# Kernel tuning notes

Measured on AMD Instinct MI355X. Metric: run time of the kernel, lower is better.

Reference implementation:

```python
import jax, jax.numpy as jnp
import numpy as np

MARGIN = 0.2
BATCH = 512
FEAT = 256
NUM_CLASSES = 64


def setup_inputs() -> dict:
    key = jax.random.key(0)
    k1, k2 = jax.random.split(key)
    inputs = jax.random.normal(k1, (BATCH, FEAT), dtype=jnp.float32)
    y = jax.random.randint(k2, (BATCH,), 0, NUM_CLASSES, dtype=jnp.int64)
    return {"inputs": inputs, "y": y}


def reference(inputs, y):
    b = y.shape[0]
    # pairwise squared distances: |x_i|^2 + |x_j|^2 - 2 x_i . x_j
    gram = inputs @ inputs.T                      # [B, B]
    sq = jnp.diagonal(gram)                       # [B]
    pdist = sq[:, None] + sq[None, :] - 2.0 * gram  # [B, B]

    # validity mask over (i, j, k): i!=j, i!=k, j!=k, y_i==y_j, y_i!=y_k
    not_eq = 1.0 - jnp.eye(b, dtype=inputs.dtype)           # [B, B]
    eq_label = (y[None, :] == y[:, None]).astype(inputs.dtype)  # [B, B]
    not_equal = (not_eq[:, :, None] * not_eq[None, :, :] * not_eq[:, None, :])
    valid_labels = eq_label[:, :, None] * (1.0 - eq_label[:, None, :])
    mask = not_equal * valid_labels                          # [B, B, B]

    num_valid = mask.sum()
    hinge = jnp.maximum((pdist[:, :, None] - pdist[:, None, :] + MARGIN) * mask, 0.0)
    return hinge.sum() / num_valid
```

## Files before the change

kernel.cpp:

```cpp
#include <hip/hip_runtime.h>

#define MARGIN 0.2f
#define BATCH 512
#define FEAT 256

__global__ __launch_bounds__(256) void pdist_kernel(const float* __restrict__ X,
                                                    float* __restrict__ pdist,
                                                    float* __restrict__ acc) {
    __shared__ float Xi[16][260];
    __shared__ float Xj[16][260];
    const int tx = threadIdx.x, ty = threadIdx.y;
    const int tid = ty * 16 + tx;
    const int i0 = blockIdx.y * 16, j0 = blockIdx.x * 16;

    const float4* X4 = (const float4*)X;
#pragma unroll
    for (int c = 0; c < 4; ++c) {
        int idx = tid + c * 256;
        int row = idx >> 6;
        int col = idx & 63;
        float4 vi = X4[(i0 + row) * 64 + col];
        float4 vj = X4[(j0 + row) * 64 + col];
        *(float4*)&Xi[row][col * 4] = vi;
        *(float4*)&Xj[row][col * 4] = vj;
    }
    __syncthreads();

    float s = 0.f;
#pragma unroll 8
    for (int f = 0; f < FEAT; ++f) {
        float d = Xi[ty][f] - Xj[tx][f];
        s = fmaf(d, d, s);
    }
    pdist[(i0 + ty) * BATCH + (j0 + tx)] = s;

    if (tid == 0 && blockIdx.x == 0 && blockIdx.y == 0) {
        acc[0] = 0.f;
        acc[1] = 0.f;
    }
}

__global__ __launch_bounds__(256) void triplet_kernel(const float* __restrict__ pdist,
                                                      const int* __restrict__ y,
                                                      float* __restrict__ acc) {
    __shared__ float pos_s[BATCH];
    __shared__ float neg_s[BATCH];
    __shared__ int   cnt_s[2];
    __shared__ float wsum[4];

    const int i = blockIdx.x;
    const int tid = threadIdx.x;
    if (tid < 2) cnt_s[tid] = 0;
    __syncthreads();

    const int yi = y[i];
    const float* drow = pdist + (size_t)i * BATCH;
    for (int j = tid; j < BATCH; j += 256) {
        int yj = y[j];
        float dj = drow[j];
        if (yj != yi) {
            int n = atomicAdd(&cnt_s[1], 1);
            neg_s[n] = dj;
        } else if (j != i) {
            int p = atomicAdd(&cnt_s[0], 1);
            pos_s[p] = dj + MARGIN;
        }
    }
    __syncthreads();

    const int cp = cnt_s[0], cn = cnt_s[1];
    float s = 0.f;
    for (int jj = 0; jj < cp; ++jj) {
        float dp = pos_s[jj];
        for (int k = tid; k < cn; k += 256) {
            s += fmaxf(dp - neg_s[k], 0.f);
        }
    }

#pragma unroll
    for (int off = 32; off > 0; off >>= 1) s += __shfl_down(s, off);
    if ((tid & 63) == 0) wsum[tid >> 6] = s;
    __syncthreads();
    if (tid == 0) {
        float bs = wsum[0] + wsum[1] + wsum[2] + wsum[3];
        atomicAdd(&acc[0], bs);
        atomicAdd(&acc[1], (float)(cp * cn));
    }
}

__global__ void finalize_kernel(const float* __restrict__ acc, float* __restrict__ out) {
    out[0] = acc[0] / acc[1];
}

extern "C" void kernel_launch(void* const* d_in, const int* in_sizes, int n_in,
                              void* d_out, int out_size, void* d_ws, size_t ws_size,
                              hipStream_t stream) {
    const float* X = (const float*)d_in[0];
    const int*   y = (const int*)d_in[1];
    float* out = (float*)d_out;

    float* pdist = (float*)d_ws;
    float* acc   = pdist + (size_t)BATCH * BATCH;

    dim3 gA(BATCH / 16, BATCH / 16), bA(16, 16);
    pdist_kernel<<<gA, bA, 0, stream>>>(X, pdist, acc);

    triplet_kernel<<<BATCH, 256, 0, stream>>>(pdist, y, acc);

    finalize_kernel<<<1, 1, 0, stream>>>(acc, out);
}
```

Baseline: 79.12 us.

## Fuse pairwise distance into per-anchor triplet kernel and use deterministic reduction

Each anchor block now computes its own row of squared distances directly from X, with one thread per candidate j, instead of going through a separate tiled pdist kernel and a global distance matrix. Positive and negative compaction uses wave ballots with one shared atomic per wave rather than one atomic per element. Per-anchor partial sums go to a buffer that a single-block reduce kernel combines, which replaces the global float atomics and the finalize launch. The trade-off is that X is reread by every anchor block without shared-memory tiling, and each thread reads a separate row with strided, uncoalesced loads, so the distance phase may be slower even though a launch and the matrix round trip are gone.

```diff
diff --git a/kernel.cpp b/kernel.cpp
--- a/kernel.cpp
+++ b/kernel.cpp
@@ -3,93 +3,99 @@
 #define MARGIN 0.2f
 #define BATCH 512
 #define FEAT 256
+#define NF4 (FEAT / 4)
 
-__global__ __launch_bounds__(256) void pdist_kernel(const float* __restrict__ X,
-                                                    float* __restrict__ pdist,
-                                                    float* __restrict__ acc) {
-    __shared__ float Xi[16][260];
-    __shared__ float Xj[16][260];
-    const int tx = threadIdx.x, ty = threadIdx.y;
-    const int tid = ty * 16 + tx;
-    const int i0 = blockIdx.y * 16, j0 = blockIdx.x * 16;
+__global__ __launch_bounds__(512) void anchor_kernel(const float* __restrict__ X,
+                                                     const int* __restrict__ y,
+                                                     float2* __restrict__ partial) {
+    __shared__ float4 xi_s[NF4];
+    __shared__ float  pos_s[BATCH];
+    __shared__ float  neg_s[BATCH];
+    __shared__ int    cnt_s[2];
+    __shared__ float  wsum[8];
 
+    const int i   = blockIdx.x;
+    const int tid = threadIdx.x;
     const float4* X4 = (const float4*)X;
-#pragma unroll
-    for (int c = 0; c < 4; ++c) {
-        int idx = tid + c * 256;
-        int row = idx >> 6;
-        int col = idx & 63;
-        float4 vi = X4[(i0 + row) * 64 + col];
-        float4 vj = X4[(j0 + row) * 64 + col];
-        *(float4*)&Xi[row][col * 4] = vi;
-        *(float4*)&Xj[row][col * 4] = vj;
-    }
+
+    if (tid < NF4) xi_s[tid] = X4[i * NF4 + tid];
+    if (tid < 2)   cnt_s[tid] = 0;
     __syncthreads();
 
     float s = 0.f;
-#pragma unroll 8
-    for (int f = 0; f < FEAT; ++f) {
-        float d = Xi[ty][f] - Xj[tx][f];
-        s = fmaf(d, d, s);
+    {
+        const float4* xj = X4 + (size_t)tid * NF4;
+#pragma unroll 4
+        for (int f = 0; f < NF4; ++f) {
+            float4 a = xi_s[f];
+            float4 b = xj[f];
+            float d0 = a.x - b.x, d1 = a.y - b.y;
+            float d2 = a.z - b.z, d3 = a.w - b.w;
+            s = fmaf(d0, d0, s); s = fmaf(d1, d1, s);
+            s = fmaf(d2, d2, s); s = fmaf(d3, d3, s);
+        }
     }
-    pdist[(i0 + ty) * BATCH + (j0 + tx)] = s;
 
-    if (tid == 0 && blockIdx.x == 0 && blockIdx.y == 0) {
-        acc[0] = 0.f;
-        acc[1] = 0.f;
+    const int yi = y[i];
+    const int yj = y[tid];
+    const bool is_pos = (yj == yi) && (tid != i);
+    const bool is_neg = (yj != yi);
+
+    const int lane = tid & 63;
+    const unsigned long long lt = (((unsigned long long)1) << lane) - 1;
+    unsigned long long mp = __ballot(is_pos);
+    unsigned long long mn = __ballot(is_neg);
+    int basep = 0, basen = 0;
+    if (lane == 0) {
+        basep = atomicAdd(&cnt_s[0], __popcll(mp));
+        basen = atomicAdd(&cnt_s[1], __popcll(mn));
+    }
+    basep = __shfl(basep, 0);
+    basen = __shfl(basen, 0);
+    if (is_pos) pos_s[basep + __popcll(mp & lt)] = s + MARGIN;
+    if (is_neg) neg_s[basen + __popcll(mn & lt)] = s;
+    __syncthreads();
+
+    const int cp = cnt_s[0], cn = cnt_s[1];
+
+    float hs = 0.f;
+    for (int jj = 0; jj < cp; ++jj) {
+        float dp = pos_s[jj];
+        for (int k = tid; k < cn; k += 512)
+            hs += fmaxf(dp - neg_s[k], 0.f);
+    }
+
+#pragma unroll
+    for (int off = 32; off > 0; off >>= 1) hs += __shfl_down(hs, off);
+    if (lane == 0) wsum[tid >> 6] = hs;
+    __syncthreads();
+    if (tid == 0) {
+        float bs = 0.f;
+#pragma unroll
+        for (int w = 0; w < 8; ++w) bs += wsum[w];
+        partial[i] = make_float2(bs, (float)(cp * cn));
     }
 }
 
-__global__ __launch_bounds__(256) void triplet_kernel(const float* __restrict__ pdist,
-                                                      const int* __restrict__ y,
-                                                      float* __restrict__ acc) {
-    __shared__ float pos_s[BATCH];
-    __shared__ float neg_s[BATCH];
-    __shared__ int   cnt_s[2];
-    __shared__ float wsum[4];
-
-    const int i = blockIdx.x;
+__global__ __launch_bounds__(512) void reduce_kernel(const float2* __restrict__ partial,
+                                                     float* __restrict__ out) {
+    __shared__ float ws[8], wc[8];
     const int tid = threadIdx.x;
-    if (tid < 2) cnt_s[tid] = 0;
-    __syncthreads();
-
-    const int yi = y[i];
-    const float* drow = pdist + (size_t)i * BATCH;
-    for (int j = tid; j < BATCH; j += 256) {
-        int yj = y[j];
-        float dj = drow[j];
-        if (yj != yi) {
-            int n = atomicAdd(&cnt_s[1], 1);
-            neg_s[n] = dj;
-        } else if (j != i) {
-            int p = atomicAdd(&cnt_s[0], 1);
-            pos_s[p] = dj + MARGIN;
-        }
+    float2 v = partial[tid];
+    float s = v.x, c = v.y;
+#pragma unroll
+    for (int off = 32; off > 0; off >>= 1) {
+        s += __shfl_down(s, off);
+        c += __shfl_down(c, off);
     }
-    __syncthreads();
-
-    const int cp = cnt_s[0], cn = cnt_s[1];
-    float s = 0.f;
-    for (int jj = 0; jj < cp; ++jj) {
-        float dp = pos_s[jj];
-        for (int k = tid; k < cn; k += 256) {
-            s += fmaxf(dp - neg_s[k], 0.f);
-        }
-    }
-
-#pragma unroll
-    for (int off = 32; off > 0; off >>= 1) s += __shfl_down(s, off);
-    if ((tid & 63) == 0) wsum[tid >> 6] = s;
+    if ((tid & 63) == 0) { ws[tid >> 6] = s; wc[tid >> 6] = c; }
     __syncthreads();
     if (tid == 0) {
-        float bs = wsum[0] + wsum[1] + wsum[2] + wsum[3];
-        atomicAdd(&acc[0], bs);
-        atomicAdd(&acc[1], (float)(cp * cn));
+        float st = 0.f, ct = 0.f;
+#pragma unroll
+        for (int w = 0; w < 8; ++w) { st += ws[w]; ct += wc[w]; }
+        out[0] = st / ct;
     }
-}
-
-__global__ void finalize_kernel(const float* __restrict__ acc, float* __restrict__ out) {
-    out[0] = acc[0] / acc[1];
 }
 
 extern "C" void kernel_launch(void* const* d_in, const int* in_sizes, int n_in,
@@ -98,14 +104,8 @@
     const float* X = (const float*)d_in[0];
     const int*   y = (const int*)d_in[1];
     float* out = (float*)d_out;
+    float2* partial = (float2*)d_ws;
 
-    float* pdist = (float*)d_ws;
-    float* acc   = pdist + (size_t)BATCH * BATCH;
-
-    dim3 gA(BATCH / 16, BATCH / 16), bA(16, 16);
-    pdist_kernel<<<gA, bA, 0, stream>>>(X, pdist, acc);
-
-    triplet_kernel<<<BATCH, 256, 0, stream>>>(pdist, y, acc);
-
-    finalize_kernel<<<1, 1, 0, stream>>>(acc, out);
+    anchor_kernel<<<BATCH, 512, 0, stream>>>(X, y, partial);
+    reduce_kernel<<<1, 512, 0, stream>>>(partial, out);
 }
```

Result: slower. 86.07 us (+8.8%).
